# Performance work log

Measured on AMD Instinct MI355X. Metric: run time of the kernel, lower is better.

The kernel has to match this reference:

```python
import jax, jax.numpy as jnp
import numpy as np

GRID_SHAPE = (32, 32)
TEMPERATURE = 1.0


def setup_inputs() -> dict:
    key = jax.random.key(0)
    k1, k2 = jax.random.split(key)
    x = jax.random.normal(k1, (16384, 1024), dtype=jnp.float32)
    som_weights = jax.random.normal(k2, (*GRID_SHAPE, 1024), dtype=jnp.float32) * 0.05
    return {"x": x, "som_weights": som_weights}


def reference(x, som_weights):
    # x: [B, D]; som_weights: [G1, G2, D]
    B, D = x.shape
    g1, g2 = GRID_SHAPE
    w_flat = som_weights.reshape(g1 * g2, D)  # [N, D]
    x_sq = jnp.sum(x * x, axis=-1, keepdims=True)          # [B, 1]
    w_sq = jnp.sum(w_flat * w_flat, axis=-1)[None, :]       # [1, N]
    d2 = x_sq - 2.0 * (x @ w_flat.T) + w_sq                 # [B, N]
    logits = (-d2 / TEMPERATURE).reshape(B, g1, g2)         # [B, G1, G2]
    # per-dimension softmax along each spatial axis, combined multiplicatively
    s1 = jax.nn.softmax(logits, axis=1)
    s2 = jax.nn.softmax(logits, axis=2)
    combined = s1 * s2
    combined = combined / (jnp.sum(combined, axis=(1, 2), keepdims=True) + 1e-8)
    # soft reconstruction: weighted sum over grid of codebook vectors
    recon = jnp.einsum('bn,nd->bd', combined.reshape(B, g1 * g2), w_flat)
    return recon
```

## Files before the change

### kernel.cpp

```cpp
#include <hip/hip_runtime.h>

static constexpr int BATCH = 16384;
static constexpr int DIM   = 1024;
static constexpr int NN    = 1024;

typedef _Float16 half8  __attribute__((ext_vector_type(8)));
typedef _Float16 half4v __attribute__((ext_vector_type(4)));
typedef float    f32x4  __attribute__((ext_vector_type(4)));

static constexpr float L2E = 1.44269504088896340736f;

__global__ __launch_bounds__(256) void prep_pack_kernel(const float* __restrict__ W,
                                                        _Float16* __restrict__ P1,
                                                        _Float16* __restrict__ P2) {
    const int l = threadIdx.x & 63;
    const int v = threadIdx.x >> 6;
    const int f = blockIdx.x * 4 + v;
    const int hi = f >> 5, lo = f & 31;
    {
        int n  = hi * 16 + (l & 15);
        int k0 = lo * 32 + (l >> 4) * 8;
        const float* src = W + (size_t)n * DIM + k0;
        f32x4 a = *(const f32x4*)src;
        f32x4 b = *(const f32x4*)(src + 4);
        half8 h;
#pragma unroll
        for (int q = 0; q < 4; ++q) { h[q] = (_Float16)a[q]; h[4 + q] = (_Float16)b[q]; }
        *(half8*)(P1 + ((size_t)f * 64 + l) * 8) = h;
    }
    {
        int d  = hi * 16 + (l & 15);
        int n0 = lo * 32 + (l >> 4) * 8;
        half8 h;
#pragma unroll
        for (int j = 0; j < 8; ++j) h[j] = (_Float16)W[(size_t)(n0 + j) * DIM + d];
        *(half8*)(P2 + ((size_t)f * 64 + l) * 8) = h;
    }
}

__global__ __launch_bounds__(256) void wsq_kernel(const float* __restrict__ W,
                                                  float* __restrict__ wsq) {
    const int n = blockIdx.x;
    const int t = threadIdx.x;
    float4 v = *(const float4*)(W + (size_t)n * DIM + 4 * t);
    float ss = v.x * v.x + v.y * v.y + v.z * v.z + v.w * v.w;
#pragma unroll
    for (int o = 32; o > 0; o >>= 1) ss += __shfl_xor(ss, o, 64);
    __shared__ float red[4];
    if ((t & 63) == 0) red[t >> 6] = ss;
    __syncthreads();
    if (t == 0) wsq[n] = L2E * (red[0] + red[1] + red[2] + red[3]);
}

__global__ __launch_bounds__(1024, 4) void fused_som_kernel(
    const float* __restrict__ X, const _Float16* __restrict__ P1,
    const _Float16* __restrict__ P2, const float* __restrict__ wsq,
    float* __restrict__ Out) {

    __shared__ __align__(16) _Float16 xs[2][64 * 64];
    __shared__ __align__(16) char     BIG[131072];
    __shared__ __align__(16) float    a1_lds[64 * 32];
    __shared__ __align__(16) float    rowred[16 * 64];
    __shared__ __align__(16) float    rowinv[64];

    const int t  = threadIdx.x;
    const int l  = t & 63;
    const int w  = t >> 6;
    const int r0 = blockIdx.x * 64;

    auto RIDX = [](int wv, int row, int g2) {
        return (wv * 64 + row) * 32 + (g2 ^ ((row & 4) << 2));
    };
    auto AIDX = [](int row, int g2) {
        return row * 32 + (g2 ^ ((row & 4) << 2));
    };

    const int srow = t >> 4;
    const int skq  = t & 15;

    auto xload = [&](int kt) -> f32x4 {
        return __builtin_nontemporal_load(
            (const f32x4*)(X + (size_t)(r0 + srow) * DIM + kt + skq * 4));
    };
    auto xwrite = [&](int buf, f32x4 v) {
        half4v h;
        h[0] = (_Float16)v[0]; h[1] = (_Float16)v[1];
        h[2] = (_Float16)v[2]; h[3] = (_Float16)v[3];
        int c = skq >> 1;
        *(half4v*)&xs[buf][srow * 64 + ((c ^ (srow & 7)) << 3) + ((skq & 1) << 2)] = h;
    };

    f32x4 acc[4][4] = {};
    {
        f32x4 xv = xload(0);
        xwrite(0, xv);
    }
    __syncthreads();

    for (int kt = 0; kt < DIM; kt += 64) {
        const int cur = (kt >> 6) & 1;
        const bool hasNext = (kt + 64 < DIM);
        f32x4 xv;
        if (hasNext) xv = xload(kt + 64);

        const int tk0 = kt >> 5;
        half8 bf0[4], bf1[4];
#pragma unroll
        for (int ni = 0; ni < 4; ++ni) {
            const size_t fb = (size_t)(w * 4 + ni) * 32;
            bf0[ni] = *(const half8*)(P1 + ((fb + tk0) * 64 + l) * 8);
            bf1[ni] = *(const half8*)(P1 + ((fb + tk0 + 1) * 64 + l) * 8);
        }
        half8 af[4];
#pragma unroll
        for (int mi = 0; mi < 4; ++mi) {
            const _Float16* pa = &xs[cur][((l & 15) + mi * 16) * 64];
            af[mi] = *(const half8*)(pa + (((l >> 4)) ^ (l & 7)) * 8);
        }
        __builtin_amdgcn_s_setprio(1);
#pragma unroll
        for (int mi = 0; mi < 4; ++mi)
#pragma unroll
            for (int ni = 0; ni < 4; ++ni)
                acc[mi][ni] = __builtin_amdgcn_mfma_f32_16x16x32_f16(
                    af[mi], bf0[ni], acc[mi][ni], 0, 0, 0);
        __builtin_amdgcn_s_setprio(0);
#pragma unroll
        for (int mi = 0; mi < 4; ++mi) {
            const _Float16* pa = &xs[cur][((l & 15) + mi * 16) * 64];
            af[mi] = *(const half8*)(pa + ((4 + (l >> 4)) ^ (l & 7)) * 8);
        }
        __builtin_amdgcn_s_setprio(1);
#pragma unroll
        for (int mi = 0; mi < 4; ++mi)
#pragma unroll
            for (int ni = 0; ni < 4; ++ni)
                acc[mi][ni] = __builtin_amdgcn_mfma_f32_16x16x32_f16(
                    af[mi], bf1[ni], acc[mi][ni], 0, 0, 0);
        __builtin_amdgcn_s_setprio(0);
        __builtin_amdgcn_sched_barrier(0);
        if (hasNext) xwrite(cur ^ 1, xv);
        __syncthreads();
    }

    float wq[4];
#pragma unroll
    for (int ni = 0; ni < 4; ++ni) wq[ni] = wsq[w * 64 + ni * 16 + (l & 15)];
#pragma unroll
    for (int mi = 0; mi < 4; ++mi)
#pragma unroll
        for (int ni = 0; ni < 4; ++ni)
#pragma unroll
            for (int q = 0; q < 4; ++q)
                acc[mi][ni][q] = exp2f(fmaf(acc[mi][ni][q], 2.0f * L2E, -wq[ni]));

    f32x4 rS2[4][2];
#pragma unroll
    for (int mi = 0; mi < 4; ++mi)
#pragma unroll
        for (int p = 0; p < 2; ++p) {
#pragma unroll
            for (int q = 0; q < 4; ++q) {
                float s = acc[mi][2 * p][q] + acc[mi][2 * p + 1][q];
                s += __shfl_xor(s, 1, 64);
                s += __shfl_xor(s, 2, 64);
                s += __shfl_xor(s, 4, 64);
                s += __shfl_xor(s, 8, 64);
                rS2[mi][p][q] = __builtin_amdgcn_rcpf(s);
            }
        }

    float* red = (float*)BIG;
#pragma unroll
    for (int mi = 0; mi < 4; ++mi)
#pragma unroll
        for (int j = 0; j < 2; ++j)
#pragma unroll
            for (int q = 0; q < 4; ++q) {
                int row = mi * 16 + (l >> 4) * 4 + q;
                red[RIDX(w, row, j * 16 + (l & 15))] =
                    acc[mi][j][q] + acc[mi][2 + j][q];
            }
    __syncthreads();
#pragma unroll
    for (int i = 0; i < 2; ++i) {
        int pr = t + i * 1024;
        int row = pr >> 5, g2 = pr & 31;
        float s = 0.f;
#pragma unroll
        for (int wv = 0; wv < 16; ++wv) s += red[RIDX(wv, row, g2)];
        a1_lds[AIDX(row, g2)] = __builtin_amdgcn_rcpf(s);
    }
    __syncthreads();

    _Float16* cs = (_Float16*)BIG;
#pragma unroll
    for (int mi = 0; mi < 4; ++mi) {
        f32x4 rs = {0.f, 0.f, 0.f, 0.f};
#pragma unroll
        for (int j = 0; j < 2; ++j) {
            f32x4 a1v;
#pragma unroll
            for (int q = 0; q < 4; ++q) {
                int row = mi * 16 + (l >> 4) * 4 + q;
                a1v[q] = a1_lds[AIDX(row, j * 16 + (l & 15))];
            }
#pragma unroll
            for (int p = 0; p < 2; ++p) {
                int ni  = 2 * p + j;
                int col = w * 64 + ni * 16 + (l & 15);
                int chunk = col >> 3;
#pragma unroll
                for (int q = 0; q < 4; ++q) {
                    float e = acc[mi][ni][q];
                    float cu = ((e * e) * a1v[q]) * rS2[mi][p][q];
                    rs[q] += cu;
                    int row = mi * 16 + (l >> 4) * 4 + q;
                    cs[row * 1024 + ((chunk ^ (row & 7)) << 3) + (col & 7)] =
                        (_Float16)cu;
                }
            }
        }
#pragma unroll
        for (int q = 0; q < 4; ++q) {
            float sv = rs[q];
            sv += __shfl_xor(sv, 1, 64);
            sv += __shfl_xor(sv, 2, 64);
            sv += __shfl_xor(sv, 4, 64);
            sv += __shfl_xor(sv, 8, 64);
            if ((l & 15) == 0) rowred[w * 64 + mi * 16 + (l >> 4) * 4 + q] = sv;
        }
    }
    __syncthreads();

    if (t < 64) {
        float tot = 0.f;
#pragma unroll
        for (int wv = 0; wv < 16; ++wv) tot += rowred[wv * 64 + t];
        rowinv[t] = 1.f / (tot + 1e-8f);
    }

    f32x4 acc2[4][4] = {};
#pragma unroll 2
    for (int kt = 0; kt < NN; kt += 32) {
        const int tn = kt >> 5;
        half8 bf[4], af2[4];
#pragma unroll
        for (int ni = 0; ni < 4; ++ni)
            bf[ni] = *(const half8*)(P2 +
                (((size_t)(w * 4 + ni) * 32 + tn) * 64 + l) * 8);
#pragma unroll
        for (int mi = 0; mi < 4; ++mi) {
            int row = (l & 15) + mi * 16;
            int kc  = tn * 4 + (l >> 4);
            af2[mi] = *(const half8*)(cs + row * 1024 + ((kc ^ (row & 7)) << 3));
        }
        __builtin_amdgcn_s_setprio(1);
#pragma unroll
        for (int mi = 0; mi < 4; ++mi)
#pragma unroll
            for (int ni = 0; ni < 4; ++ni)
                acc2[mi][ni] = __builtin_amdgcn_mfma_f32_16x16x32_f16(
                    af2[mi], bf[ni], acc2[mi][ni], 0, 0, 0);
        __builtin_amdgcn_s_setprio(0);
    }

    __syncthreads();
    float* stg = (float*)BIG;
#pragma unroll
    for (int half = 0; half < 2; ++half) {
        if (half) __syncthreads();
#pragma unroll
        for (int mm = 0; mm < 2; ++mm) {
            const int mi = half * 2 + mm;
#pragma unroll
            for (int ni = 0; ni < 4; ++ni) {
                const int col = w * 64 + ni * 16 + (l & 15);
#pragma unroll
                for (int q = 0; q < 4; ++q) {
                    const int rr = (l >> 4) * 4 + q;
                    const float inv = rowinv[mi * 16 + rr];
                    stg[(mm * 16 + rr) * 1024 + (col ^ ((rr & 4) << 2))] =
                        acc2[mi][ni][q] * inv;
                }
            }
        }
        __syncthreads();
#pragma unroll
        for (int i = 0; i < 8; ++i) {
            const int c  = t + i * 1024;
            const int rr = c >> 8;
            const int c4 = c & 255;
            f32x4 v = *(const f32x4*)&stg[rr * 1024 + ((c4 * 4) ^ ((rr & 4) << 2))];
            __builtin_nontemporal_store(v,
                (f32x4*)(Out + (size_t)(r0 + half * 32 + rr) * DIM + c4 * 4));
        }
    }
}

extern "C" void kernel_launch(void* const* d_in, const int* in_sizes, int n_in,
                              void* d_out, int out_size, void* d_ws, size_t ws_size,
                              hipStream_t stream) {
    const float* x = (const float*)d_in[0];
    const float* w = (const float*)d_in[1];
    float* out = (float*)d_out;

    char* ws = (char*)d_ws;
    size_t off = 0;
    _Float16* pack1 = (_Float16*)(ws + off); off += (size_t)NN * DIM * 2;
    _Float16* pack2 = (_Float16*)(ws + off); off += (size_t)DIM * NN * 2;
    float*    wsq   = (float*)   (ws + off); off += (size_t)NN * 4;

    prep_pack_kernel<<<512, 256, 0, stream>>>(w, pack1, pack2);
    wsq_kernel<<<NN, 256, 0, stream>>>(w, wsq);
    fused_som_kernel<<<BATCH / 64, 1024, 0, stream>>>(x, pack1, pack2, wsq, out);
}
```

Before: 203.3 us.

## Prefetch packed W fragments one step ahead and store output directly

Both GEMM loops now load the B-operand fragments (P1/P2) from global memory one k-step ahead into registers, so the load latency overlaps the current MFMA block instead of stalling at the start of each iteration. The second GEMM uses an explicit double buffer of B fragments. The LDS-staged, coalesced 16-byte nontemporal output store is replaced by per-element scalar global stores straight from the accumulators, which removes two barriers and the LDS round trip. The cost is more live registers, which may lower occupancy or cause spills, and poorly coalesced 4-byte output writes.

```diff
diff --git a/kernel.cpp b/kernel.cpp
--- a/kernel.cpp
+++ b/kernel.cpp
@@ -89,12 +89,21 @@
         int c = skq >> 1;
         *(half4v*)&xs[buf][srow * 64 + ((c ^ (srow & 7)) << 3) + ((skq & 1) << 2)] = h;
     };
+    auto loadB1 = [&](int tk, half8* dst) {
+#pragma unroll
+        for (int ni = 0; ni < 4; ++ni)
+            dst[ni] = *(const half8*)(P1 +
+                (((size_t)(w * 4 + ni) * 32 + tk) * 64 + l) * 8);
+    };
 
     f32x4 acc[4][4] = {};
     {
         f32x4 xv = xload(0);
         xwrite(0, xv);
     }
+    half8 bf0[4], bf1[4];
+    loadB1(0, bf0);
+    loadB1(1, bf1);
     __syncthreads();
 
     for (int kt = 0; kt < DIM; kt += 64) {
@@ -102,15 +111,8 @@
         const bool hasNext = (kt + 64 < DIM);
         f32x4 xv;
         if (hasNext) xv = xload(kt + 64);
-
-        const int tk0 = kt >> 5;
-        half8 bf0[4], bf1[4];
-#pragma unroll
-        for (int ni = 0; ni < 4; ++ni) {
-            const size_t fb = (size_t)(w * 4 + ni) * 32;
-            bf0[ni] = *(const half8*)(P1 + ((fb + tk0) * 64 + l) * 8);
-            bf1[ni] = *(const half8*)(P1 + ((fb + tk0 + 1) * 64 + l) * 8);
-        }
+        const int tkn = (kt >> 5) + 2;
+
         half8 af[4];
 #pragma unroll
         for (int mi = 0; mi < 4; ++mi) {
@@ -125,6 +127,7 @@
                 acc[mi][ni] = __builtin_amdgcn_mfma_f32_16x16x32_f16(
                     af[mi], bf0[ni], acc[mi][ni], 0, 0, 0);
         __builtin_amdgcn_s_setprio(0);
+        if (hasNext) loadB1(tkn, bf0);
 #pragma unroll
         for (int mi = 0; mi < 4; ++mi) {
             const _Float16* pa = &xs[cur][((l & 15) + mi * 16) * 64];
@@ -138,6 +141,7 @@
                 acc[mi][ni] = __builtin_amdgcn_mfma_f32_16x16x32_f16(
                     af[mi], bf1[ni], acc[mi][ni], 0, 0, 0);
         __builtin_amdgcn_s_setprio(0);
+        if (hasNext) loadB1(tkn + 1, bf1);
         __builtin_amdgcn_sched_barrier(0);
         if (hasNext) xwrite(cur ^ 1, xv);
         __syncthreads();
@@ -240,62 +244,56 @@
         rowinv[t] = 1.f / (tot + 1e-8f);
     }
 
-    f32x4 acc2[4][4] = {};
-#pragma unroll 2
-    for (int kt = 0; kt < NN; kt += 32) {
-        const int tn = kt >> 5;
-        half8 bf[4], af2[4];
+    auto loadB2 = [&](int tn, half8* dst) {
 #pragma unroll
         for (int ni = 0; ni < 4; ++ni)
-            bf[ni] = *(const half8*)(P2 +
+            dst[ni] = *(const half8*)(P2 +
                 (((size_t)(w * 4 + ni) * 32 + tn) * 64 + l) * 8);
+    };
+    auto ldA2 = [&](int tn, half8* dst) {
 #pragma unroll
         for (int mi = 0; mi < 4; ++mi) {
             int row = (l & 15) + mi * 16;
             int kc  = tn * 4 + (l >> 4);
-            af2[mi] = *(const half8*)(cs + row * 1024 + ((kc ^ (row & 7)) << 3));
-        }
+            dst[mi] = *(const half8*)(cs + row * 1024 + ((kc ^ (row & 7)) << 3));
+        }
+    };
+    auto mfma16 = [&](f32x4 (&a2)[4][4], half8* af2, half8* bf) {
         __builtin_amdgcn_s_setprio(1);
 #pragma unroll
         for (int mi = 0; mi < 4; ++mi)
 #pragma unroll
             for (int ni = 0; ni < 4; ++ni)
-                acc2[mi][ni] = __builtin_amdgcn_mfma_f32_16x16x32_f16(
-                    af2[mi], bf[ni], acc2[mi][ni], 0, 0, 0);
+                a2[mi][ni] = __builtin_amdgcn_mfma_f32_16x16x32_f16(
+                    af2[mi], bf[ni], a2[mi][ni], 0, 0, 0);
         __builtin_amdgcn_s_setprio(0);
-    }
-
-    __syncthreads();
-    float* stg = (float*)BIG;
-#pragma unroll
-    for (int half = 0; half < 2; ++half) {
-        if (half) __syncthreads();
-#pragma unroll
-        for (int mm = 0; mm < 2; ++mm) {
-            const int mi = half * 2 + mm;
+    };
+
+    f32x4 acc2[4][4] = {};
+    half8 bfA[4], bfB[4], af2[4];
+    loadB2(0, bfA);
+    for (int tn = 0; tn < 32; tn += 2) {
+        if (tn + 1 < 32) loadB2(tn + 1, bfB);
+        ldA2(tn, af2);
+        mfma16(acc2, af2, bfA);
+        if (tn + 2 < 32) loadB2(tn + 2, bfA);
+        ldA2(tn + 1, af2);
+        mfma16(acc2, af2, bfB);
+    }
+    __syncthreads();
+
+#pragma unroll
+    for (int mi = 0; mi < 4; ++mi)
+#pragma unroll
+        for (int q = 0; q < 4; ++q) {
+            const int rr  = mi * 16 + (l >> 4) * 4 + q;
+            const float inv = rowinv[rr];
 #pragma unroll
             for (int ni = 0; ni < 4; ++ni) {
                 const int col = w * 64 + ni * 16 + (l & 15);
-#pragma unroll
-                for (int q = 0; q < 4; ++q) {
-                    const int rr = (l >> 4) * 4 + q;
-                    const float inv = rowinv[mi * 16 + rr];
-                    stg[(mm * 16 + rr) * 1024 + (col ^ ((rr & 4) << 2))] =
-                        acc2[mi][ni][q] * inv;
-                }
-            }
-        }
-        __syncthreads();
-#pragma unroll
-        for (int i = 0; i < 8; ++i) {
-            const int c  = t + i * 1024;
-            const int rr = c >> 8;
-            const int c4 = c & 255;
-            f32x4 v = *(const f32x4*)&stg[rr * 1024 + ((c4 * 4) ^ ((rr & 4) << 2))];
-            __builtin_nontemporal_store(v,
-                (f32x4*)(Out + (size_t)(r0 + half * 32 + rr) * DIM + c4 * 4));
-        }
-    }
+                Out[(size_t)(r0 + rr) * DIM + col] = acc2[mi][ni][q] * inv;
+            }
+        }
 }
 
 extern "C" void kernel_launch(void* const* d_in, const int* in_sizes, int n_in,
```

Result: slower. 270.3 us (+33.0%).
